# Kernel tuning notes

Hardware: AMD Instinct MI355X
Metric: run time of the kernel (lower is better)

## Reference

```python
import jax, jax.numpy as jnp
import numpy as np

B, S, D, F, E = 4, 1024, 768, 3072, 8


def setup_inputs() -> dict:
    key = jax.random.key(0)
    k0, k1, k2, k3 = jax.random.split(key, 4)
    hidden_states = jax.random.normal(k0, (B, S, D), dtype=jnp.float32)
    w_router = jax.random.normal(k1, (D, E), dtype=jnp.float32) * 0.02
    w1 = jax.random.normal(k2, (E, D, F), dtype=jnp.float32) * 0.02
    b1 = jnp.zeros((E, F), dtype=jnp.float32)
    w2 = jax.random.normal(k3, (E, F, D), dtype=jnp.float32) * 0.02
    b2 = jnp.zeros((E, D), dtype=jnp.float32)
    return {"hidden_states": hidden_states, "w_router": w_router,
            "w1": w1, "b1": b1, "w2": w2, "b2": b2}


def reference(hidden_states, w_router, w1, b1, w2, b2):
    # Switch-style top-1 router: logits -> softmax -> one-hot mask + max prob
    router_logits = jnp.einsum("bsd,de->bse", hidden_states, w_router)
    router_probs_full = jax.nn.softmax(router_logits, axis=-1)
    expert_index = jnp.argmax(router_probs_full, axis=-1)            # [B,S] int
    router_probs = jnp.max(router_probs_full, axis=-1, keepdims=True)  # [B,S,1]
    router_mask = jax.nn.one_hot(expert_index, E, dtype=hidden_states.dtype)  # [B,S,E]

    # Dispatch/compute/combine: each token goes to exactly one expert FFN.
    # Loop over the small fixed expert set (E=8), combine via the one-hot mask;
    # math is identical to the gather -> expert FFN -> scatter of the original.
    out = jnp.zeros_like(hidden_states)
    for e in range(E):
        h = jax.nn.relu(jnp.einsum("bsd,df->bsf", hidden_states, w1[e]) + b1[e])
        h = jnp.einsum("bsf,fd->bsd", h, w2[e]) + b2[e]
        out = out + router_mask[..., e:e + 1] * h

    hidden_out = router_probs * out  # scale by top-1 router prob, as in original
    return hidden_out, router_logits, expert_index
```

## Files before the change

kernel.cpp:

```cpp
#include <hip/hip_runtime.h>
#include <hip/hip_bf16.h>

#define T_TOK 4096
#define DIM   768
#define FF    3072
#define NE    8

typedef __attribute__((ext_vector_type(8))) short bf16x8;
typedef __attribute__((ext_vector_type(4))) short bf16x4;
typedef __attribute__((ext_vector_type(4))) float f32x4;
typedef __attribute__((ext_vector_type(2))) float f32x2;

typedef __attribute__((address_space(1))) void gvoid_t;
typedef __attribute__((address_space(3))) void lvoid_t;

__device__ __forceinline__ void g2l16(const void* g, void* l) {
    __builtin_amdgcn_global_load_lds((gvoid_t*)(void*)g, (lvoid_t*)l, 16, 0, 0);
}

#define WAIT_VM0() __builtin_amdgcn_s_waitcnt(0x0F70)
#define RAW_BARRIER() asm volatile("s_barrier" ::: "memory")

__device__ __forceinline__ unsigned short f2bf(float f) {
    union { float f; unsigned int u; } v; v.f = f;
    unsigned int u = v.u;
    u += 0x7FFFu + ((u >> 16) & 1u);
    return (unsigned short)(u >> 16);
}

__device__ __forceinline__ bf16x8 pack8(f32x4 a, f32x4 b) {
    bf16x8 r;
    r[0] = (short)f2bf(a[0]); r[1] = (short)f2bf(a[1]);
    r[2] = (short)f2bf(a[2]); r[3] = (short)f2bf(a[3]);
    r[4] = (short)f2bf(b[0]); r[5] = (short)f2bf(b[1]);
    r[6] = (short)f2bf(b[2]); r[7] = (short)f2bf(b[3]);
    return r;
}

__global__ __launch_bounds__(256) void k_router(
    const float* __restrict__ x, const float* __restrict__ wr,
    float* __restrict__ out_logits, float* __restrict__ out_eidx,
    float* __restrict__ probs, int* __restrict__ eidx_i,
    int* __restrict__ counts, int* __restrict__ bucket)
{
    int tok  = (blockIdx.x * 256 + threadIdx.x) >> 6;
    int lane = threadIdx.x & 63;
    if (tok >= T_TOK) return;
    const float* xr = x + (size_t)tok * DIM;
    float acc[NE];
    #pragma unroll
    for (int e = 0; e < NE; e++) acc[e] = 0.f;
    #pragma unroll
    for (int j = 0; j < DIM / 64; j++) {
        int d = j * 64 + lane;
        float xv = xr[d];
        const float* wrow = wr + (size_t)d * NE;
        #pragma unroll
        for (int e = 0; e < NE; e++) acc[e] += xv * wrow[e];
    }
    #pragma unroll
    for (int e = 0; e < NE; e++) {
        #pragma unroll
        for (int off = 32; off >= 1; off >>= 1)
            acc[e] += __shfl_xor(acc[e], off);
    }
    if (lane == 0) {
        float mx = acc[0]; int mi = 0;
        #pragma unroll
        for (int e = 1; e < NE; e++) if (acc[e] > mx) { mx = acc[e]; mi = e; }
        float se = 0.f;
        #pragma unroll
        for (int e = 0; e < NE; e++) se += __expf(acc[e] - mx);
        #pragma unroll
        for (int e = 0; e < NE; e++) out_logits[(size_t)tok * NE + e] = acc[e];
        out_eidx[tok] = (float)mi;
        eidx_i[tok] = mi;
        probs[tok] = 1.f / se;
        int pos = atomicAdd(&counts[mi], 1);
        bucket[mi * T_TOK + pos] = tok;
    }
}

__global__ void k_compact(const int* __restrict__ counts, int* __restrict__ offsets,
                          const int* __restrict__ bucket, int* __restrict__ sorted)
{
    __shared__ int soff[NE + 1];
    if (threadIdx.x == 0) {
        int s = 0;
        for (int e = 0; e < NE; e++) { soff[e] = s; s += counts[e]; }
        soff[NE] = s;
        for (int e = 0; e <= NE; e++) offsets[e] = soff[e];
    }
    __syncthreads();
    for (int e = 0; e < NE; e++) {
        int c = counts[e], o = soff[e];
        for (int i = threadIdx.x; i < c; i += blockDim.x)
            sorted[o + i] = bucket[e * T_TOK + i];
    }
}

__global__ __launch_bounds__(256) void k_xconv(
    const float* __restrict__ x, unsigned short* __restrict__ Xb)
{
    int g0 = (blockIdx.x * 256 + threadIdx.x) * 8;
    if (g0 >= T_TOK * DIM) return;
    f32x4 a = *(const f32x4*)(x + g0);
    f32x4 b = *(const f32x4*)(x + g0 + 4);
    *(bf16x8*)(Xb + g0) = pack8(a, b);
}

__global__ __launch_bounds__(256) void k_tconv(
    const float* __restrict__ in, unsigned short* __restrict__ out, int R, int C)
{
    const size_t es = (size_t)R * C;
    in  += blockIdx.z * es;
    out += blockIdx.z * es;
    const int c0 = blockIdx.x * 64, r0 = blockIdx.y * 64;
    __shared__ unsigned short t[64][72];
    const int tr = threadIdx.x >> 2, tc = (threadIdx.x & 3) * 16;
    const float* src = in + (size_t)(r0 + tr) * C + c0 + tc;
    f32x4 v0 = *(const f32x4*)(src);
    f32x4 v1 = *(const f32x4*)(src + 4);
    f32x4 v2 = *(const f32x4*)(src + 8);
    f32x4 v3 = *(const f32x4*)(src + 12);
    const int xb = (tc >> 4) & 3;
    const int pr = (((tr >> 3) ^ xb) & 7) * 8 + (tr & 7);
    #pragma unroll
    for (int j = 0; j < 4; j++) {
        t[tc + j][pr]      = f2bf(v0[j]);
        t[tc + 4 + j][pr]  = f2bf(v1[j]);
        t[tc + 8 + j][pr]  = f2bf(v2[j]);
        t[tc + 12 + j][pr] = f2bf(v3[j]);
    }
    __syncthreads();
    const int oc = threadIdx.x >> 2, orr = (threadIdx.x & 3) * 16;
    const int rx = (oc >> 4) & 3;
    const int p0 = ((((orr >> 3) + 0) ^ rx) & 7) * 8;
    const int p1 = ((((orr >> 3) + 1) ^ rx) & 7) * 8;
    bf16x8 o0 = *(const bf16x8*)&t[oc][p0];
    bf16x8 o1 = *(const bf16x8*)&t[oc][p1];
    unsigned short* dst = out + (size_t)(c0 + oc) * R + r0 + orr;
    *(bf16x8*)(dst)     = o0;
    *(bf16x8*)(dst + 8) = o1;
}

__global__ __launch_bounds__(256) void k_init(
    const float* __restrict__ b2, const int* __restrict__ eidx,
    const float* __restrict__ probs, float* __restrict__ outh)
{
    int tok = blockIdx.x;
    int e = eidx[tok];
    float p = probs[tok];
    const float* br = b2 + e * DIM;
    for (int d = threadIdx.x; d < DIM; d += 256)
        outh[(size_t)tok * DIM + d] = br[d] * p;
}

__global__ __launch_bounds__(256, 4) void k_gemm1(
    const unsigned short* __restrict__ Xb, const unsigned short* __restrict__ wt1,
    const float* __restrict__ b1, const int* __restrict__ sorted,
    const int* __restrict__ counts, const int* __restrict__ offsets,
    unsigned short* __restrict__ Hbuf)
{
    const int e  = blockIdx.y >> 5;
    const int ti = blockIdx.y & 31;
    const int cnt = counts[e];
    if (ti * 128 >= cnt) return;
    const int n0 = blockIdx.x * 128;
    const int off = offsets[e];
    const int rbase = ti * 128;
    const int tid = threadIdx.x, lane = tid & 63, wave = tid >> 6;
    const int wm = wave >> 1, wn = wave & 1;

    __shared__ unsigned short As[2][128][32];
    __shared__ unsigned short Bs[2][128][32];

    const int lr = lane >> 2;
    const int ls = (lane & 3) * 8;

    int r0 = rbase + wave * 32 + lr;        if (r0 >= cnt) r0 = rbase;
    int r1 = rbase + wave * 32 + 16 + lr;   if (r1 >= cnt) r1 = rbase;
    const unsigned short* aP0 = Xb + (size_t)sorted[off + r0] * DIM + ls;
    const unsigned short* aP1 = Xb + (size_t)sorted[off + r1] * DIM + ls;
    const unsigned short* wB  = wt1 + (size_t)e * FF * DIM;
    const unsigned short* bP0 = wB + (size_t)(n0 + wave * 32 + lr) * DIM + ls;
    const unsigned short* bP1 = wB + (size_t)(n0 + wave * 32 + 16 + lr) * DIM + ls;

    f32x4 acc[4][4];
    #pragma unroll
    for (int i = 0; i < 4; i++)
        #pragma unroll
        for (int j = 0; j < 4; j++) acc[i][j] = (f32x4)0.f;

    const int lrow = lane & 15, kq = lane >> 4;
    const int NIT = DIM / 32;

    g2l16(aP0, &As[0][wave * 32][0]);
    g2l16(aP1, &As[0][wave * 32 + 16][0]);
    g2l16(bP0, &Bs[0][wave * 32][0]);
    g2l16(bP1, &Bs[0][wave * 32 + 16][0]);

    for (int it = 0; it < NIT; ++it) {
        const int buf = it & 1;
        if (it == 0) {
            __syncthreads();
        } else {
            WAIT_VM0();
            RAW_BARRIER();
        }
        if (it + 1 < NIT) {
            const int nb_ = (it + 1) & 1;
            const int ko = (it + 1) * 32;
            g2l16(aP0 + ko, &As[nb_][wave * 32][0]);
            g2l16(aP1 + ko, &As[nb_][wave * 32 + 16][0]);
            g2l16(bP0 + ko, &Bs[nb_][wave * 32][0]);
            g2l16(bP1 + ko, &Bs[nb_][wave * 32 + 16][0]);
        }
        bf16x8 af[4], bfv[4];
        #pragma unroll
        for (int i = 0; i < 4; i++)
            af[i] = *(const bf16x8*)&As[buf][wm * 64 + i * 16 + lrow][kq * 8];
        #pragma unroll
        for (int i = 0; i < 4; i++)
            bfv[i] = *(const bf16x8*)&Bs[buf][wn * 64 + i * 16 + lrow][kq * 8];
        #pragma unroll
        for (int mi = 0; mi < 4; mi++)
            #pragma unroll
            for (int ni = 0; ni < 4; ni++)
                acc[mi][ni] = __builtin_amdgcn_mfma_f32_16x16x32_bf16(
                    af[mi], bfv[ni], acc[mi][ni], 0, 0, 0);
    }

    const int quad = lane >> 4;
    #pragma unroll
    for (int ni = 0; ni < 4; ni++) {
        int gn = n0 + wn * 64 + ni * 16 + lrow;
        float bias = b1[e * FF + gn];
        #pragma unroll
        for (int mi = 0; mi < 4; mi++) {
            f32x4 v = acc[mi][ni];
            #pragma unroll
            for (int r = 0; r < 4; r++) {
                int ml = rbase + wm * 64 + mi * 16 + quad * 4 + r;
                if (ml < cnt) {
                    float h = v[r] + bias; h = h > 0.f ? h : 0.f;
                    Hbuf[(size_t)(off + ml) * FF + gn] = f2bf(h);
                }
            }
        }
    }
}

__global__ __launch_bounds__(256, 4) void k_gemm2(
    const unsigned short* __restrict__ Hbuf, const unsigned short* __restrict__ wt2,
    const int* __restrict__ sorted, const int* __restrict__ counts,
    const int* __restrict__ offsets, const float* __restrict__ probs,
    float* __restrict__ outh)
{
    const int e  = blockIdx.y >> 5;
    const int ti = blockIdx.y & 31;
    const int cnt = counts[e];
    if (ti * 128 >= cnt) return;
    const int n0 = blockIdx.x * 128;
    const int kc = blockIdx.z;
    const int off = offsets[e];
    const int rbase = ti * 128;
    const int tid = threadIdx.x, lane = tid & 63, wave = tid >> 6;
    const int wm = wave >> 1, wn = wave & 1;

    __shared__ unsigned short As[2][128][32];
    __shared__ unsigned short Bs[2][128][32];
    __shared__ int   s_tok[128];
    __shared__ float s_prob[128];

    if (tid < 128) {
        int rr = rbase + tid; if (rr >= cnt) rr = rbase;
        int tk = sorted[off + rr];
        s_tok[tid]  = tk;
        s_prob[tid] = probs[tk];
    }

    const int lr = lane >> 2, ls = (lane & 3) * 8;
    int r0 = rbase + wave * 32 + lr;        if (r0 >= cnt) r0 = rbase;
    int r1 = rbase + wave * 32 + 16 + lr;   if (r1 >= cnt) r1 = rbase;
    const unsigned short* aP0 = Hbuf + (size_t)(off + r0) * FF + kc * 768 + ls;
    const unsigned short* aP1 = Hbuf + (size_t)(off + r1) * FF + kc * 768 + ls;
    const unsigned short* wB  = wt2 + (size_t)e * DIM * FF;
    const unsigned short* bP0 = wB + (size_t)(n0 + wave * 32 + lr) * FF + kc * 768 + ls;
    const unsigned short* bP1 = wB + (size_t)(n0 + wave * 32 + 16 + lr) * FF + kc * 768 + ls;

    f32x4 acc[4][4];
    #pragma unroll
    for (int i = 0; i < 4; i++)
        #pragma unroll
        for (int j = 0; j < 4; j++) acc[i][j] = (f32x4)0.f;

    const int lrow = lane & 15, kq = lane >> 4;
    const int NIT = 768 / 32;

    g2l16(aP0, &As[0][wave * 32][0]);
    g2l16(aP1, &As[0][wave * 32 + 16][0]);
    g2l16(bP0, &Bs[0][wave * 32][0]);
    g2l16(bP1, &Bs[0][wave * 32 + 16][0]);

    for (int it = 0; it < NIT; ++it) {
        const int buf = it & 1;
        if (it == 0) {
            __syncthreads();
        } else {
            WAIT_VM0();
            RAW_BARRIER();
        }
        if (it + 1 < NIT) {
            const int nb_ = (it + 1) & 1;
            const int ko = (it + 1) * 32;
            g2l16(aP0 + ko, &As[nb_][wave * 32][0]);
            g2l16(aP1 + ko, &As[nb_][wave * 32 + 16][0]);
            g2l16(bP0 + ko, &Bs[nb_][wave * 32][0]);
            g2l16(bP1 + ko, &Bs[nb_][wave * 32 + 16][0]);
        }
        bf16x8 af[4], bfv[4];
        #pragma unroll
        for (int i = 0; i < 4; i++)
            af[i] = *(const bf16x8*)&As[buf][wm * 64 + i * 16 + lrow][kq * 8];
        #pragma unroll
        for (int i = 0; i < 4; i++)
            bfv[i] = *(const bf16x8*)&Bs[buf][wn * 64 + i * 16 + lrow][kq * 8];
        #pragma unroll
        for (int mi = 0; mi < 4; mi++)
            #pragma unroll
            for (int ni = 0; ni < 4; ni++)
                acc[mi][ni] = __builtin_amdgcn_mfma_f32_16x16x32_bf16(
                    af[mi], bfv[ni], acc[mi][ni], 0, 0, 0);
    }

    const int quad = lane >> 4;
    #pragma unroll
    for (int ni = 0; ni < 4; ni++) {
        int gn = n0 + wn * 64 + ni * 16 + lrow;
        #pragma unroll
        for (int mi = 0; mi < 4; mi++) {
            f32x4 v = acc[mi][ni];
            #pragma unroll
            for (int r = 0; r < 4; r++) {
                int mloc = wm * 64 + mi * 16 + quad * 4 + r;
                if (rbase + mloc < cnt) {
                    atomicAdd(&outh[(size_t)s_tok[mloc] * DIM + gn], v[r] * s_prob[mloc]);
                }
            }
        }
    }
}

__global__ __launch_bounds__(256) void k_gather_fb(
    const float* __restrict__ x, const int* __restrict__ sorted,
    unsigned short* __restrict__ Xg)
{
    int g0 = (blockIdx.x * 256 + threadIdx.x) * 8;
    if (g0 >= T_TOK * DIM) return;
    int row = g0 / DIM, col = g0 - row * DIM;
    const float* src = x + (size_t)sorted[row] * DIM + col;
    f32x4 a = *(const f32x4*)(src);
    f32x4 b = *(const f32x4*)(src + 4);
    *(bf16x8*)(Xg + (size_t)row * DIM + col) = pack8(a, b);
}

__global__ __launch_bounds__(256, 3) void k_gemm1_fb(
    const unsigned short* __restrict__ Xg, const float* __restrict__ w1,
    const float* __restrict__ b1, const int* __restrict__ counts,
    const int* __restrict__ offsets, unsigned short* __restrict__ Hbuf)
{
    const int e   = blockIdx.y >> 5;
    const int ti  = blockIdx.y & 31;
    const int cnt = counts[e];
    if (ti * 128 >= cnt) return;
    const int n0    = blockIdx.x * 128;
    const int off   = offsets[e];
    const int rbase = ti * 128;
    const int rmax  = cnt - rbase - 1;
    const int tid   = threadIdx.x;
    const int lane  = tid & 63;
    const int wave  = tid >> 6;
    const int wm = wave >> 1, wn = wave & 1;
    __shared__ unsigned short As[128][72];
    __shared__ unsigned short Bs[128][72];
    const float* w1e = w1 + (size_t)e * DIM * FF;
    f32x4 acc[4][4];
    #pragma unroll
    for (int i = 0; i < 4; i++)
        #pragma unroll
        for (int j = 0; j < 4; j++) acc[i][j] = (f32x4)0.f;
    const int arow = tid >> 1, aseg = tid & 1;
    const int are  = (arow <= rmax) ? arow : 0;
    const unsigned short* abase = Xg + (size_t)(off + rbase + are) * DIM + aseg * 32;
    const int kb = tid >> 5, nb = tid & 31;
    const float* bbase = w1e + (size_t)kb * 8 * FF + n0 + nb * 4;
    bf16x8 aR[4];
    f32x4  bR[8];
    #pragma unroll
    for (int j = 0; j < 4; j++) aR[j] = *(const bf16x8*)(abase + j * 8);
    #pragma unroll
    for (int r = 0; r < 8; r++) bR[r] = *(const f32x4*)(bbase + (size_t)r * FF);
    const int lrow = lane & 15, kq = lane >> 4;
    for (int it = 0; it < DIM / 64; ++it) {
        __syncthreads();
        #pragma unroll
        for (int j = 0; j < 4; j++)
            *(bf16x8*)&As[arow][aseg * 32 + j * 8] = aR[j];
        #pragma unroll
        for (int j = 0; j < 4; j++) {
            bf16x8 c;
            #pragma unroll
            for (int r = 0; r < 8; r++) c[r] = (short)f2bf(bR[r][j]);
            *(bf16x8*)&Bs[nb * 4 + j][kb * 8] = c;
        }
        __syncthreads();
        if (it + 1 < DIM / 64) {
            const unsigned short* an = abase + (it + 1) * 64;
            #pragma unroll
            for (int j = 0; j < 4; j++) aR[j] = *(const bf16x8*)(an + j * 8);
            const float* bn = bbase + (size_t)(it + 1) * 64 * FF;
            #pragma unroll
            for (int r = 0; r < 8; r++) bR[r] = *(const f32x4*)(bn + (size_t)r * FF);
        }
        #pragma unroll
        for (int ks = 0; ks < 2; ks++) {
            bf16x8 af[4], bfr[4];
            #pragma unroll
            for (int i = 0; i < 4; i++)
                af[i] = *(const bf16x8*)&As[wm * 64 + i * 16 + lrow][ks * 32 + kq * 8];
            #pragma unroll
            for (int i = 0; i < 4; i++)
                bfr[i] = *(const bf16x8*)&Bs[wn * 64 + i * 16 + lrow][ks * 32 + kq * 8];
            #pragma unroll
            for (int mi = 0; mi < 4; mi++)
                #pragma unroll
                for (int ni = 0; ni < 4; ni++)
                    acc[mi][ni] = __builtin_amdgcn_mfma_f32_16x16x32_bf16(
                        af[mi], bfr[ni], acc[mi][ni], 0, 0, 0);
        }
    }
    const int quad = lane >> 4;
    #pragma unroll
    for (int ni = 0; ni < 4; ni++) {
        int gn = n0 + wn * 64 + ni * 16 + lrow;
        float bias = b1[e * FF + gn];
        #pragma unroll
        for (int mi = 0; mi < 4; mi++) {
            f32x4 v = acc[mi][ni];
            #pragma unroll
            for (int r = 0; r < 4; r++) {
                int ml = wm * 64 + mi * 16 + quad * 4 + r;
                if (rbase + ml < cnt) {
                    float h = v[r] + bias;
                    h = h > 0.f ? h : 0.f;
                    Hbuf[(size_t)(off + rbase + ml) * FF + gn] = f2bf(h);
                }
            }
        }
    }
}

__global__ __launch_bounds__(256, 4) void k_gemm2_fb(
    const unsigned short* __restrict__ Hbuf, const float* __restrict__ w2,
    const float* __restrict__ b2, const int* __restrict__ sorted,
    const int* __restrict__ counts, const int* __restrict__ offsets,
    const float* __restrict__ probs, float* __restrict__ outh)
{
    const int e   = blockIdx.y >> 5;
    const int ti  = blockIdx.y & 31;
    const int cnt = counts[e];
    if (ti * 128 >= cnt) return;
    const int n0    = blockIdx.x * 64;
    const int off   = offsets[e];
    const int rbase = ti * 128;
    const int rmax  = cnt - rbase - 1;
    const int tid   = threadIdx.x;
    const int lane  = tid & 63;
    const int wave  = tid >> 6;
    const int wm = wave >> 1, wn = wave & 1;
    __shared__ unsigned short As[128][72];
    __shared__ unsigned short Bs[64][72];
    __shared__ int   s_tok[128];
    __shared__ float s_prob[128];
    if (tid < 128) {
        int r = rbase + tid;
        int tk = sorted[off + ((r < cnt) ? r : rbase)];
        s_tok[tid]  = tk;
        s_prob[tid] = probs[tk];
    }
    const float* w2e = w2 + (size_t)e * FF * DIM;
    f32x4 acc[4][2];
    #pragma unroll
    for (int i = 0; i < 4; i++)
        #pragma unroll
        for (int j = 0; j < 2; j++) acc[i][j] = (f32x4)0.f;
    const int arow = tid >> 1, aseg = tid & 1;
    const int are  = (arow <= rmax) ? arow : 0;
    const unsigned short* abase = Hbuf + (size_t)(off + rbase + are) * FF + aseg * 32;
    const int kb = tid >> 5, nb = tid & 31;
    const float* bbase = w2e + (size_t)kb * 8 * DIM + n0 + nb * 2;
    bf16x8 aR[4];
    f32x2  bR[8];
    #pragma unroll
    for (int j = 0; j < 4; j++) aR[j] = *(const bf16x8*)(abase + j * 8);
    #pragma unroll
    for (int r = 0; r < 8; r++) bR[r] = *(const f32x2*)(bbase + (size_t)r * DIM);
    const int lrow = lane & 15, kq = lane >> 4;
    for (int it = 0; it < FF / 64; ++it) {
        __syncthreads();
        #pragma unroll
        for (int j = 0; j < 4; j++)
            *(bf16x8*)&As[arow][aseg * 32 + j * 8] = aR[j];
        {
            bf16x8 c0, c1;
            #pragma unroll
            for (int r = 0; r < 8; r++) { c0[r] = (short)f2bf(bR[r][0]); c1[r] = (short)f2bf(bR[r][1]); }
            *(bf16x8*)&Bs[nb * 2 + 0][kb * 8] = c0;
            *(bf16x8*)&Bs[nb * 2 + 1][kb * 8] = c1;
        }
        __syncthreads();
        if (it + 1 < FF / 64) {
            const unsigned short* an = abase + (it + 1) * 64;
            #pragma unroll
            for (int j = 0; j < 4; j++) aR[j] = *(const bf16x8*)(an + j * 8);
            const float* bn = bbase + (size_t)(it + 1) * 64 * DIM;
            #pragma unroll
            for (int r = 0; r < 8; r++) bR[r] = *(const f32x2*)(bn + (size_t)r * DIM);
        }
        #pragma unroll
        for (int ks = 0; ks < 2; ks++) {
            bf16x8 af[4], bfr[2];
            #pragma unroll
            for (int i = 0; i < 4; i++)
                af[i] = *(const bf16x8*)&As[wm * 64 + i * 16 + lrow][ks * 32 + kq * 8];
            #pragma unroll
            for (int i = 0; i < 2; i++)
                bfr[i] = *(const bf16x8*)&Bs[wn * 32 + i * 16 + lrow][ks * 32 + kq * 8];
            #pragma unroll
            for (int mi = 0; mi < 4; mi++)
                #pragma unroll
                for (int ni = 0; ni < 2; ni++)
                    acc[mi][ni] = __builtin_amdgcn_mfma_f32_16x16x32_bf16(
                        af[mi], bfr[ni], acc[mi][ni], 0, 0, 0);
        }
    }
    const int quad = lane >> 4;
    #pragma unroll
    for (int ni = 0; ni < 2; ni++) {
        int gn = n0 + wn * 32 + ni * 16 + lrow;
        float bias = b2[e * DIM + gn];
        #pragma unroll
        for (int mi = 0; mi < 4; mi++) {
            f32x4 v = acc[mi][ni];
            #pragma unroll
            for (int r = 0; r < 4; r++) {
                int ml = wm * 64 + mi * 16 + quad * 4 + r;
                if (rbase + ml < cnt) {
                    outh[(size_t)s_tok[ml] * DIM + gn] = (v[r] + bias) * s_prob[ml];
                }
            }
        }
    }
}

extern "C" void kernel_launch(void* const* d_in, const int* in_sizes, int n_in,
                              void* d_out, int out_size, void* d_ws, size_t ws_size,
                              hipStream_t stream) {
    (void)in_sizes; (void)n_in; (void)out_size;
    const float* x  = (const float*)d_in[0];
    const float* wr = (const float*)d_in[1];
    const float* w1 = (const float*)d_in[2];
    const float* b1 = (const float*)d_in[3];
    const float* w2 = (const float*)d_in[4];
    const float* b2 = (const float*)d_in[5];

    float* out_hidden = (float*)d_out;
    float* out_logits = out_hidden + (size_t)T_TOK * DIM;
    float* out_eidx   = out_logits + (size_t)T_TOK * NE;

    char* ws = (char*)d_ws;
    int*   counts  = (int*)(ws + 0);
    int*   offsets = (int*)(ws + 64);
    float* probs   = (float*)(ws + 128);
    int*   eidx_i  = (int*)(ws + 16512);
    int*   sorted  = (int*)(ws + 32896);
    int*   bucket  = (int*)(ws + 49280);
    unsigned short* Xb   = (unsigned short*)(ws + 180352);
    unsigned short* Hbuf = (unsigned short*)(ws + 6471808);
    unsigned short* wt1  = (unsigned short*)(ws + 31637632);
    unsigned short* wt2  = (unsigned short*)(ws + 69386368);
    const size_t NEED = 107135104;

    hipMemsetAsync(counts, 0, 32, stream);
    k_router<<<dim3(T_TOK / 4), dim3(256), 0, stream>>>(
        x, wr, out_logits, out_eidx, probs, eidx_i, counts, bucket);
    k_compact<<<dim3(1), dim3(256), 0, stream>>>(counts, offsets, bucket, sorted);

    if (ws_size >= NEED) {
        k_xconv<<<dim3(T_TOK * DIM / 8 / 256), dim3(256), 0, stream>>>(x, Xb);
        k_tconv<<<dim3(FF / 64, DIM / 64, NE), dim3(256), 0, stream>>>(w1, wt1, DIM, FF);
        k_tconv<<<dim3(DIM / 64, FF / 64, NE), dim3(256), 0, stream>>>(w2, wt2, FF, DIM);
        k_init<<<dim3(T_TOK), dim3(256), 0, stream>>>(b2, eidx_i, probs, out_hidden);
        k_gemm1<<<dim3(FF / 128, NE * 32), dim3(256), 0, stream>>>(
            Xb, wt1, b1, sorted, counts, offsets, Hbuf);
        k_gemm2<<<dim3(DIM / 128, NE * 32, 4), dim3(256), 0, stream>>>(
            Hbuf, wt2, sorted, counts, offsets, probs, out_hidden);
    } else {
        k_gather_fb<<<dim3(T_TOK * DIM / 8 / 256), dim3(256), 0, stream>>>(x, sorted, Xb);
        k_gemm1_fb<<<dim3(FF / 128, NE * 32), dim3(256), 0, stream>>>(
            Xb, w1, b1, counts, offsets, Hbuf);
        k_gemm2_fb<<<dim3(DIM / 64, NE * 32), dim3(256), 0, stream>>>(
            Hbuf, w2, b2, sorted, counts, offsets, probs, out_hidden);
    }
}
```

Before: 394.4 us.

## Triple-buffer GEMM loads and replace split-K atomics with partial buffers plus reduce

Both expert GEMMs now use three LDS stages, prefetching two K-steps ahead with a partial vmcnt wait, so global-to-LDS loads overlap more of the MFMA work. GEMM2 drops from a 4-way to a 3-way K split and writes plain partial sums into a scratch buffer (placed over the wt1 region, which is dead by then). A new finish kernel sums the three partials, adds the bias and scales by the router probability, replacing the init kernel and the float atomics. The cost is more LDS per block with lower occupancy bounds, one extra pass over the output, and reliance on that workspace aliasing being safe.

```diff
diff --git a/kernel.cpp b/kernel.cpp
--- a/kernel.cpp
+++ b/kernel.cpp
@@ -19,6 +19,7 @@
 }
 
 #define WAIT_VM0() __builtin_amdgcn_s_waitcnt(0x0F70)
+#define WAIT_VM4() __builtin_amdgcn_s_waitcnt(0x0F74)
 #define RAW_BARRIER() asm volatile("s_barrier" ::: "memory")
 
 __device__ __forceinline__ unsigned short f2bf(float f) {
@@ -144,19 +145,24 @@
     *(bf16x8*)(dst + 8) = o1;
 }
 
-__global__ __launch_bounds__(256) void k_init(
-    const float* __restrict__ b2, const int* __restrict__ eidx,
-    const float* __restrict__ probs, float* __restrict__ outh)
-{
-    int tok = blockIdx.x;
-    int e = eidx[tok];
-    float p = probs[tok];
+__global__ __launch_bounds__(256) void k_fin(
+    const float* __restrict__ P, const float* __restrict__ b2,
+    const int* __restrict__ eidx, const float* __restrict__ probs,
+    float* __restrict__ outh)
+{
+    const int tok = blockIdx.x;
+    const float p = probs[tok];
+    const int e = eidx[tok];
+    const float* p0 = P + (size_t)tok * DIM;
+    const float* p1 = p0 + (size_t)T_TOK * DIM;
+    const float* p2 = p1 + (size_t)T_TOK * DIM;
     const float* br = b2 + e * DIM;
+    float* o = outh + (size_t)tok * DIM;
     for (int d = threadIdx.x; d < DIM; d += 256)
-        outh[(size_t)tok * DIM + d] = br[d] * p;
-}
-
-__global__ __launch_bounds__(256, 4) void k_gemm1(
+        o[d] = p * (p0[d] + p1[d] + p2[d] + br[d]);
+}
+
+__global__ __launch_bounds__(256, 3) void k_gemm1(
     const unsigned short* __restrict__ Xb, const unsigned short* __restrict__ wt1,
     const float* __restrict__ b1, const int* __restrict__ sorted,
     const int* __restrict__ counts, const int* __restrict__ offsets,
@@ -172,8 +178,8 @@
     const int tid = threadIdx.x, lane = tid & 63, wave = tid >> 6;
     const int wm = wave >> 1, wn = wave & 1;
 
-    __shared__ unsigned short As[2][128][32];
-    __shared__ unsigned short Bs[2][128][32];
+    __shared__ unsigned short As[3][128][32];
+    __shared__ unsigned short Bs[3][128][32];
 
     const int lr = lane >> 2;
     const int ls = (lane & 3) * 8;
@@ -199,18 +205,21 @@
     g2l16(aP1, &As[0][wave * 32 + 16][0]);
     g2l16(bP0, &Bs[0][wave * 32][0]);
     g2l16(bP1, &Bs[0][wave * 32 + 16][0]);
+    __syncthreads();
+    g2l16(aP0 + 32, &As[1][wave * 32][0]);
+    g2l16(aP1 + 32, &As[1][wave * 32 + 16][0]);
+    g2l16(bP0 + 32, &Bs[1][wave * 32][0]);
+    g2l16(bP1 + 32, &Bs[1][wave * 32 + 16][0]);
 
     for (int it = 0; it < NIT; ++it) {
-        const int buf = it & 1;
-        if (it == 0) {
-            __syncthreads();
-        } else {
-            WAIT_VM0();
+        const int buf = it % 3;
+        if (it > 0) {
+            WAIT_VM4();
             RAW_BARRIER();
         }
-        if (it + 1 < NIT) {
-            const int nb_ = (it + 1) & 1;
-            const int ko = (it + 1) * 32;
+        if (it + 2 < NIT) {
+            const int nb_ = (it + 2) % 3;
+            const int ko = (it + 2) * 32;
             g2l16(aP0 + ko, &As[nb_][wave * 32][0]);
             g2l16(aP1 + ko, &As[nb_][wave * 32 + 16][0]);
             g2l16(bP0 + ko, &Bs[nb_][wave * 32][0]);
@@ -251,11 +260,10 @@
     }
 }
 
-__global__ __launch_bounds__(256, 4) void k_gemm2(
+__global__ __launch_bounds__(256, 3) void k_gemm2(
     const unsigned short* __restrict__ Hbuf, const unsigned short* __restrict__ wt2,
     const int* __restrict__ sorted, const int* __restrict__ counts,
-    const int* __restrict__ offsets, const float* __restrict__ probs,
-    float* __restrict__ outh)
+    const int* __restrict__ offsets, float* __restrict__ Pbuf)
 {
     const int e  = blockIdx.y >> 5;
     const int ti = blockIdx.y & 31;
@@ -268,26 +276,23 @@
     const int tid = threadIdx.x, lane = tid & 63, wave = tid >> 6;
     const int wm = wave >> 1, wn = wave & 1;
 
-    __shared__ unsigned short As[2][128][32];
-    __shared__ unsigned short Bs[2][128][32];
-    __shared__ int   s_tok[128];
-    __shared__ float s_prob[128];
+    __shared__ unsigned short As[3][128][32];
+    __shared__ unsigned short Bs[3][128][32];
+    __shared__ int s_tok[128];
 
     if (tid < 128) {
         int rr = rbase + tid; if (rr >= cnt) rr = rbase;
-        int tk = sorted[off + rr];
-        s_tok[tid]  = tk;
-        s_prob[tid] = probs[tk];
+        s_tok[tid] = sorted[off + rr];
     }
 
     const int lr = lane >> 2, ls = (lane & 3) * 8;
     int r0 = rbase + wave * 32 + lr;        if (r0 >= cnt) r0 = rbase;
     int r1 = rbase + wave * 32 + 16 + lr;   if (r1 >= cnt) r1 = rbase;
-    const unsigned short* aP0 = Hbuf + (size_t)(off + r0) * FF + kc * 768 + ls;
-    const unsigned short* aP1 = Hbuf + (size_t)(off + r1) * FF + kc * 768 + ls;
+    const unsigned short* aP0 = Hbuf + (size_t)(off + r0) * FF + kc * 1024 + ls;
+    const unsigned short* aP1 = Hbuf + (size_t)(off + r1) * FF + kc * 1024 + ls;
     const unsigned short* wB  = wt2 + (size_t)e * DIM * FF;
-    const unsigned short* bP0 = wB + (size_t)(n0 + wave * 32 + lr) * FF + kc * 768 + ls;
-    const unsigned short* bP1 = wB + (size_t)(n0 + wave * 32 + 16 + lr) * FF + kc * 768 + ls;
+    const unsigned short* bP0 = wB + (size_t)(n0 + wave * 32 + lr) * FF + kc * 1024 + ls;
+    const unsigned short* bP1 = wB + (size_t)(n0 + wave * 32 + 16 + lr) * FF + kc * 1024 + ls;
 
     f32x4 acc[4][4];
     #pragma unroll
@@ -296,24 +301,27 @@
         for (int j = 0; j < 4; j++) acc[i][j] = (f32x4)0.f;
 
     const int lrow = lane & 15, kq = lane >> 4;
-    const int NIT = 768 / 32;
+    const int NIT = 1024 / 32;
 
     g2l16(aP0, &As[0][wave * 32][0]);
     g2l16(aP1, &As[0][wave * 32 + 16][0]);
     g2l16(bP0, &Bs[0][wave * 32][0]);
     g2l16(bP1, &Bs[0][wave * 32 + 16][0]);
+    __syncthreads();
+    g2l16(aP0 + 32, &As[1][wave * 32][0]);
+    g2l16(aP1 + 32, &As[1][wave * 32 + 16][0]);
+    g2l16(bP0 + 32, &Bs[1][wave * 32][0]);
+    g2l16(bP1 + 32, &Bs[1][wave * 32 + 16][0]);
 
     for (int it = 0; it < NIT; ++it) {
-        const int buf = it & 1;
-        if (it == 0) {
-            __syncthreads();
-        } else {
-            WAIT_VM0();
+        const int buf = it % 3;
+        if (it > 0) {
+            WAIT_VM4();
             RAW_BARRIER();
         }
-        if (it + 1 < NIT) {
-            const int nb_ = (it + 1) & 1;
-            const int ko = (it + 1) * 32;
+        if (it + 2 < NIT) {
+            const int nb_ = (it + 2) % 3;
+            const int ko = (it + 2) * 32;
             g2l16(aP0 + ko, &As[nb_][wave * 32][0]);
             g2l16(aP1 + ko, &As[nb_][wave * 32 + 16][0]);
             g2l16(bP0 + ko, &Bs[nb_][wave * 32][0]);
@@ -334,6 +342,7 @@
                     af[mi], bfv[ni], acc[mi][ni], 0, 0, 0);
     }
 
+    float* Pk = Pbuf + (size_t)kc * T_TOK * DIM;
     const int quad = lane >> 4;
     #pragma unroll
     for (int ni = 0; ni < 4; ni++) {
@@ -345,7 +354,7 @@
             for (int r = 0; r < 4; r++) {
                 int mloc = wm * 64 + mi * 16 + quad * 4 + r;
                 if (rbase + mloc < cnt) {
-                    atomicAdd(&outh[(size_t)s_tok[mloc] * DIM + gn], v[r] * s_prob[mloc]);
+                    Pk[(size_t)s_tok[mloc] * DIM + gn] = v[r];
                 }
             }
         }
@@ -590,6 +599,7 @@
     unsigned short* Hbuf = (unsigned short*)(ws + 6471808);
     unsigned short* wt1  = (unsigned short*)(ws + 31637632);
     unsigned short* wt2  = (unsigned short*)(ws + 69386368);
+    float* Pbuf = (float*)(ws + 31637632);
     const size_t NEED = 107135104;
 
     hipMemsetAsync(counts, 0, 32, stream);
@@ -601,11 +611,12 @@
         k_xconv<<<dim3(T_TOK * DIM / 8 / 256), dim3(256), 0, stream>>>(x, Xb);
         k_tconv<<<dim3(FF / 64, DIM / 64, NE), dim3(256), 0, stream>>>(w1, wt1, DIM, FF);
         k_tconv<<<dim3(DIM / 64, FF / 64, NE), dim3(256), 0, stream>>>(w2, wt2, FF, DIM);
-        k_init<<<dim3(T_TOK), dim3(256), 0, stream>>>(b2, eidx_i, probs, out_hidden);
         k_gemm1<<<dim3(FF / 128, NE * 32), dim3(256), 0, stream>>>(
             Xb, wt1, b1, sorted, counts, offsets, Hbuf);
-        k_gemm2<<<dim3(DIM / 128, NE * 32, 4), dim3(256), 0, stream>>>(
-            Hbuf, wt2, sorted, counts, offsets, probs, out_hidden);
+        k_gemm2<<<dim3(DIM / 128, NE * 32, 3), dim3(256), 0, stream>>>(
+            Hbuf, wt2, sorted, counts, offsets, Pbuf);
+        k_fin<<<dim3(T_TOK), dim3(256), 0, stream>>>(
+            Pbuf, b2, eidx_i, probs, out_hidden);
     } else {
         k_gather_fb<<<dim3(T_TOK * DIM / 8 / 256), dim3(256), 0, stream>>>(x, sorted, Xb);
         k_gemm1_fb<<<dim3(FF / 128, NE * 32), dim3(256), 0, stream>>>(
```

Measured after the change: 379.6 us. 1.04x faster.
